# Kernel optimization log

Measured on AMD Instinct MI355X. Metric: run time of the kernel, lower is better.

Reference implementation:

```python
import jax, jax.numpy as jnp
import numpy as np

T, B, V, E, H = 512, 64, 50000, 256, 256  # seq, batch, vocab, embed, lstm_hidden
D2 = 2 * H
NC = 5


def setup_inputs() -> dict:
    key = jax.random.key(0)
    ks = jax.random.split(key, 16)
    u = lambda k, shape, s=0.1: jax.random.uniform(k, shape, jnp.float32, -s, s)
    return {
        "embed": jax.random.randint(ks[0], (T, B), 0, V),
        "h0": jnp.zeros((2, B, H), jnp.float32),
        "c0": jnp.zeros((2, B, H), jnp.float32),
        "emb_table": jax.random.normal(ks[1], (V, E), jnp.float32),
        "Wih_f": u(ks[2], (4 * H, E)),
        "Whh_f": u(ks[3], (4 * H, H)),
        "bih_f": u(ks[4], (4 * H,)),
        "bhh_f": u(ks[5], (4 * H,)),
        "Wih_b": u(ks[6], (4 * H, E)),
        "Whh_b": u(ks[7], (4 * H, H)),
        "bih_b": u(ks[8], (4 * H,)),
        "bhh_b": u(ks[9], (4 * H,)),
        "W_word": u(ks[10], (D2, D2)),
        "b_word": u(ks[11], (D2,)),
        "proj_word": u(ks[12], (D2,)),
        "lin_W": u(ks[13], (NC, D2)),
        "lin_b": u(ks[14], (NC,)),
    }


def _lstm_dir(x, h0, c0, Wih, Whh, bih, bhh):
    # x: (T,B,E). PyTorch LSTM gate order: i, f, g, o.
    xg = jnp.einsum('tbe,ge->tbg', x, Wih) + bih + bhh  # (T,B,4H)

    def step(carry, xt):
        h, c = carry
        g = xt + h @ Whh.T
        i, f, gg, o = jnp.split(g, 4, axis=-1)
        c = jax.nn.sigmoid(f) * c + jax.nn.sigmoid(i) * jnp.tanh(gg)
        h = jax.nn.sigmoid(o) * jnp.tanh(c)
        return (h, c), h

    _, hs = jax.lax.scan(step, (h0, c0), xg)
    return hs  # (T,B,H)


def reference(embed, h0, c0, emb_table,
              Wih_f, Whh_f, bih_f, bhh_f,
              Wih_b, Whh_b, bih_b, bhh_b,
              W_word, b_word, proj_word, lin_W, lin_b):
    x = emb_table[embed]  # (T,B,E)
    out_f = _lstm_dir(x, h0[0], c0[0], Wih_f, Whh_f, bih_f, bhh_f)
    out_b = _lstm_dir(x[::-1], h0[1], c0[1], Wih_b, Whh_b, bih_b, bhh_b)[::-1]
    out = jnp.concatenate([out_f, out_b], axis=-1)  # (T,B,2H)
    # additive attention: tanh(out @ W + b) @ proj, softmax over T
    squish = jnp.tanh(jnp.einsum('tbd,de->tbe', out, W_word) + b_word)
    attn = jax.nn.softmax(jnp.einsum('tbd,d->tb', squish, proj_word), axis=0)
    vec = jnp.einsum('tb,tbd->bd', attn, out)  # (B,2H)
    return vec @ lin_W.T + lin_b  # (B, n_classes)
```

## Files before the change

kernel.cpp:

```cpp
#include <hip/hip_runtime.h>
#include <hip/hip_fp16.h>
#include <cstdint>
#include <cstddef>

#define TT 512
#define BB 64
#define EE 256
#define HH 256
#define G4 1024
#define DD 512
#define NCLS 5
#define CH 64
#define NCH (TT / CH)

typedef _Float16 half8 __attribute__((ext_vector_type(8)));
typedef float f32x4 __attribute__((ext_vector_type(4)));

#define OFF_XGF   0ull
#define OFF_XGB   8388608ull
#define OFF_OUTB  16777216ull
#define OFF_WHHF  50331648ull
#define OFF_WIHF  51380224ull
#define OFF_BIAS  52428800ull
#define OFF_HST   52436992ull
#define OFF_CST   52568064ull
#define OFF_LOG   52699136ull
#define OFF_ATT   52830208ull
#define OFF_HEX   52961280ull
#define OFF_FLG   53092352ull

__device__ __forceinline__ f32x4 mfma16(half8 a, half8 b, f32x4 c) {
  return __builtin_amdgcn_mfma_f32_16x16x32_f16(a, b, c, 0, 0, 0);
}
__device__ __forceinline__ float sigm(float x) {
  return __fdividef(1.f, 1.f + __expf(-x));
}
__device__ __forceinline__ float tanh_(float x) {
  float e = __expf(2.f * x);
  return 1.f - __fdividef(2.f, e + 1.f);
}
__device__ __forceinline__ f32x4 shflx4(f32x4 v, int mask) {
  f32x4 r;
  r[0] = __shfl_xor(v[0], mask, 64);
  r[1] = __shfl_xor(v[1], mask, 64);
  r[2] = __shfl_xor(v[2], mask, 64);
  r[3] = __shfl_xor(v[3], mask, 64);
  return r;
}

#define HSWZ(br, u) ((((br) * 256) + (u)) ^ (((br) & 7) << 3))

__global__ __launch_bounds__(256) void make_frags(
    const float* __restrict__ WhhF, const float* __restrict__ WhhB,
    const float* __restrict__ WihF, const float* __restrict__ WihB,
    __half* __restrict__ whhfrag, __half* __restrict__ wihfrag)
{
  int idx = blockIdx.x * 256 + threadIdx.x;
  int r = idx & 7, lane = (idx >> 3) & 63, ks = (idx >> 9) & 7;
  int mm = lane & 15;
  int k = ks * 32 + (lane >> 4) * 8 + r;
  if (idx < (1 << 19)) {
    int pf = (idx >> 12) & 63, d = (idx >> 18) & 1;
    const float* W = d ? WhhB : WhhF;
    int g = (mm & 3) * 256 + pf * 4 + (mm >> 2);
    whhfrag[idx] = __float2half(W[(size_t)g * HH + k]);
  } else {
    int e = idx - (1 << 19);
    int pf = (e >> 12) & 63, d = (e >> 18) & 1;
    const float* W = d ? WihB : WihF;
    int g = (mm & 3) * 256 + pf * 4 + (mm >> 2);
    wihfrag[e] = __float2half(W[(size_t)g * EE + k]);
  }
}

__global__ __launch_bounds__(256) void bias_prep(
    const float* __restrict__ bihF, const float* __restrict__ bhhF,
    const float* __restrict__ bihB, const float* __restrict__ bhhB,
    float* __restrict__ bias)
{
  int i = blockIdx.x * 256 + threadIdx.x;
  int d = i >> 10, pcol = i & 1023;
  int g = (pcol & 3) * 256 + (pcol >> 2);
  bias[i] = (d ? bihB : bihF)[g] + (d ? bhhB : bhhF)[g];
}

__global__ __launch_bounds__(256) void xg_mfma(
    int c, const int* __restrict__ embed, const float* __restrict__ emb,
    const __half* __restrict__ wihfrag, const float* __restrict__ biassum,
    __half* __restrict__ xgF, __half* __restrict__ xgB)
{
  const int d = blockIdx.z, ls = blockIdx.x, gblk = blockIdx.y;
  int t = c * CH + ls;
  if (d) t = TT - 1 - t;
  __half* xg = d ? xgB : xgF;
  const int tid = threadIdx.x, w = tid >> 6, l = tid & 63;

  __shared__ int idx[64];
  __shared__ unsigned short xs[64 * 256];

  if (tid < 64) idx[tid] = embed[t * BB + tid];
  __syncthreads();

  {
    const int rr = tid >> 2, cq = (tid & 3) * 64;
    const float* src = emb + (size_t)idx[rr] * EE + cq;
#pragma unroll
    for (int j = 0; j < 8; ++j) {
      float4 a = *(const float4*)(src + j * 8);
      float4 b = *(const float4*)(src + j * 8 + 4);
      half8 hv;
      hv[0] = (_Float16)a.x; hv[1] = (_Float16)a.y; hv[2] = (_Float16)a.z; hv[3] = (_Float16)a.w;
      hv[4] = (_Float16)b.x; hv[5] = (_Float16)b.y; hv[6] = (_Float16)b.z; hv[7] = (_Float16)b.w;
      int hidx = (rr * 256 + cq + j * 8) ^ ((rr & 7) << 3);
      *(half8*)&xs[hidx] = hv;
    }
  }
  __syncthreads();

  const __half* bfb = wihfrag + (size_t)((d * 64 + gblk * 4) * 8) * 512 + l * 8;
  half8 Bf[4][8];
#pragma unroll
  for (int ct = 0; ct < 4; ++ct)
#pragma unroll
    for (int ks = 0; ks < 8; ++ks)
      Bf[ct][ks] = *(const half8*)(bfb + (ct * 8 + ks) * 512);

  f32x4 acc[4];
#pragma unroll
  for (int ct = 0; ct < 4; ++ct) {
    float bv = biassum[d * 1024 + gblk * 64 + ct * 16 + (l & 15)];
    acc[ct][0] = bv; acc[ct][1] = bv; acc[ct][2] = bv; acc[ct][3] = bv;
  }

  const int arow = w * 16 + (l & 15);
#pragma unroll
  for (int ks = 0; ks < 8; ++ks) {
    int hidx = (arow * 256 + ks * 32 + (l >> 4) * 8) ^ ((arow & 7) << 3);
    half8 af = *(const half8*)&xs[hidx];
#pragma unroll
    for (int ct = 0; ct < 4; ++ct)
      acc[ct] = mfma16(af, Bf[ct][ks], acc[ct]);
  }

#pragma unroll
  for (int ct = 0; ct < 4; ++ct) {
    ushort4 sv;
    sv.x = __half_as_ushort(__float2half(acc[ct][0]));
    sv.y = __half_as_ushort(__float2half(acc[ct][1]));
    sv.z = __half_as_ushort(__float2half(acc[ct][2]));
    sv.w = __half_as_ushort(__float2half(acc[ct][3]));
    size_t base = ((size_t)(ls * 4 + w) * 64 + (gblk * 4 + ct)) * 256 + l * 4;
    *(ushort4*)((unsigned short*)xg + base) = sv;
  }
}

__global__ __launch_bounds__(512, 2) void scan_dist(
    int c, const __half* __restrict__ xgF, const __half* __restrict__ xgB,
    const __half* __restrict__ whhfrag,
    const float* __restrict__ hin, const float* __restrict__ cin,
    float* __restrict__ hstate, float* __restrict__ cstate,
    __half* __restrict__ outb, __half* __restrict__ hex, int* __restrict__ flags)
{
  const int d = blockIdx.y;
  const int bg = blockIdx.x >> 2, ug = blockIdx.x & 3;
  const int tid = threadIdx.x, w = tid >> 6, l = tid & 63;
  const int m = l & 15, qr = l >> 4, q = m & 3, ul = m >> 2;
  const unsigned short* xg = (const unsigned short*)(d ? xgB : xgF);

  __shared__ unsigned short hb[16 * 256];

  const int pf0 = ug * 16 + w * 2;

  half8 Wf[2][8];
#pragma unroll
  for (int cf = 0; cf < 2; ++cf)
#pragma unroll
    for (int ks = 0; ks < 8; ++ks)
      Wf[cf][ks] = *(const half8*)(whhfrag +
          ((size_t)(d * 64 + pf0 + cf) * 8 + ks) * 512 + l * 8);

#pragma unroll
  for (int i = 0; i < 8; ++i) {
    int idx = i * 512 + tid;
    int r = idx >> 8, u = idx & 255;
    hb[HSWZ(r, u)] = __half_as_ushort(
        __float2half(hin[(size_t)(d * BB + bg * 16 + r) * HH + u]));
  }
  float cst[2][4];
#pragma unroll
  for (int cf = 0; cf < 2; ++cf) {
    int U = (pf0 + cf) * 4 + ul;
#pragma unroll
    for (int j = 0; j < 4; ++j)
      cst[cf][j] = cin[(size_t)(d * BB + bg * 16 + qr * 4 + j) * HH + U];
  }
  __syncthreads();

  const int pr = tid >> 5;
  const int uL = (tid & 31) * 2;

  for (int ls = 0; ls < CH; ++ls) {
    int t = c * CH + ls;
    if (d) t = TT - 1 - t;

    ushort4 xv[2];
#pragma unroll
    for (int cf = 0; cf < 2; ++cf) {
      size_t base = ((size_t)(ls * 4 + bg) * 64 + (pf0 + cf)) * 256 + l * 4;
      xv[cf] = *(const ushort4*)(xg + base);
    }
    half8 af[8];
#pragma unroll
    for (int ks = 0; ks < 8; ++ks)
      af[ks] = *(const half8*)&hb[HSWZ(m, ks * 32 + qr * 8)];
    __syncthreads();

    f32x4 acc[2];
#pragma unroll
    for (int cf = 0; cf < 2; ++cf) {
      acc[cf][0] = __half2float(__ushort_as_half(xv[cf].x));
      acc[cf][1] = __half2float(__ushort_as_half(xv[cf].y));
      acc[cf][2] = __half2float(__ushort_as_half(xv[cf].z));
      acc[cf][3] = __half2float(__ushort_as_half(xv[cf].w));
    }
#pragma unroll
    for (int ks = 0; ks < 8; ++ks)
#pragma unroll
      for (int cf = 0; cf < 2; ++cf)
        acc[cf] = mfma16(af[ks], Wf[cf][ks], acc[cf]);

#pragma unroll
    for (int cf = 0; cf < 2; ++cf) {
      f32x4 e = acc[cf];
      f32x4 o1 = shflx4(e, 1);
      f32x4 gev = (q & 1) ? o1 : e;
      f32x4 gov = (q & 1) ? e : o1;
      f32x4 ge2 = shflx4(gev, 2);
      f32x4 go2 = shflx4(gov, 2);
      f32x4 gi = (q & 2) ? ge2 : gev;
      f32x4 gg = (q & 2) ? gev : ge2;
      f32x4 gf = (q & 2) ? go2 : gov;
      f32x4 go = (q & 2) ? gov : go2;
      int U = (pf0 + cf) * 4 + ul;
#pragma unroll
      for (int j = 0; j < 4; ++j) {
        float ig = sigm(gi[j]), fg = sigm(gf[j]);
        float gz = tanh_(gg[j]), og = sigm(go[j]);
        cst[cf][j] = fg * cst[cf][j] + ig * gz;
        float hv = og * tanh_(cst[cf][j]);
        if (q == 0) {
          int r = qr * 4 + j;
          hb[HSWZ(r, U)] = __half_as_ushort(__float2half(hv));
        }
      }
    }
    __syncthreads();

    unsigned int* hexu =
        (unsigned int*)hex + (size_t)(d * 2 + (ls & 1)) * (64 * 256 / 2);
    {
      int u = ug * 64 + uL;
      unsigned int v = *(const unsigned int*)&hb[HSWZ(pr, u)];
      __hip_atomic_store(&hexu[((bg * 16 + pr) * 256 + u) >> 1], v,
                         __ATOMIC_RELAXED, __HIP_MEMORY_SCOPE_AGENT);
      *(unsigned int*)&outb[((size_t)t * BB + bg * 16 + pr) * DD + d * HH + u] =
          v;
    }
    asm volatile("s_waitcnt vmcnt(0)" ::: "memory");
    __syncthreads();
    const int fbase = (((d * NCH + c) * CH + ls) * 4 + bg) * 4;
    if (tid == 0)
      __hip_atomic_store(&flags[fbase + ug], 1, __ATOMIC_RELAXED,
                         __HIP_MEMORY_SCOPE_AGENT);
    if (tid < 4 && tid != ug) {
      while (__hip_atomic_load(&flags[fbase + tid], __ATOMIC_RELAXED,
                               __HIP_MEMORY_SCOPE_AGENT) == 0)
        __builtin_amdgcn_s_sleep(1);
    }
    asm volatile("" ::: "memory");
    __syncthreads();

#pragma unroll
    for (int p = 0; p < 3; ++p) {
      int peer = p + (p >= ug ? 1 : 0);
      int u = peer * 64 + uL;
      unsigned int pv =
          __hip_atomic_load(&hexu[((bg * 16 + pr) * 256 + u) >> 1],
                            __ATOMIC_RELAXED, __HIP_MEMORY_SCOPE_AGENT);
      *(unsigned int*)&hb[HSWZ(pr, u)] = pv;
    }
    __syncthreads();
  }

#pragma unroll
  for (int i = 0; i < 8; ++i) {
    int idx = i * 512 + tid;
    int r = idx >> 8, u = idx & 255;
    hstate[(size_t)(d * BB + bg * 16 + r) * HH + u] =
        __half2float(__ushort_as_half(hb[HSWZ(r, u)]));
  }
  if (q == 0) {
#pragma unroll
    for (int cf = 0; cf < 2; ++cf) {
      int U = (pf0 + cf) * 4 + ul;
#pragma unroll
      for (int j = 0; j < 4; ++j)
        cstate[(size_t)(d * BB + bg * 16 + qr * 4 + j) * HH + U] = cst[cf][j];
    }
  }
}

__global__ __launch_bounds__(1024, 1) void squish_logits(
    const __half* __restrict__ outb, const float* __restrict__ Ww,
    const float* __restrict__ bw, const float* __restrict__ proj,
    float* __restrict__ logits)
{
  const int r0 = blockIdx.x * 64;
  const int tid = threadIdx.x;
  const int tm = tid >> 6;
  const int tn = tid & 63;
  __shared__ float As[16][68];
  __shared__ float Bs[16][516];
  __shared__ float red[64][65];

  float acc[4][8] = {};
  const int am = tid >> 4, ak = tid & 15;
  const int bk = tid >> 7, bn = (tid & 127) * 4;

  for (int k0 = 0; k0 < DD; k0 += 16) {
    float a0 = __half2float(outb[(size_t)(r0 + am) * DD + k0 + ak]);
    float4 b0 = *(const float4*)&Ww[(size_t)(k0 + bk) * DD + bn];
    float4 b1 = *(const float4*)&Ww[(size_t)(k0 + bk + 8) * DD + bn];
    __syncthreads();
    As[ak][am] = a0;
    *(float4*)&Bs[bk][bn] = b0;
    *(float4*)&Bs[bk + 8][bn] = b1;
    __syncthreads();
#pragma unroll
    for (int k = 0; k < 16; ++k) {
      float4 a = *(const float4*)&As[k][tm * 4];
      float4 p0 = *(const float4*)&Bs[k][tn * 8];
      float4 p1 = *(const float4*)&Bs[k][tn * 8 + 4];
      float av[4] = {a.x, a.y, a.z, a.w};
#pragma unroll
      for (int i = 0; i < 4; ++i) {
        acc[i][0] += av[i] * p0.x; acc[i][1] += av[i] * p0.y;
        acc[i][2] += av[i] * p0.z; acc[i][3] += av[i] * p0.w;
        acc[i][4] += av[i] * p1.x; acc[i][5] += av[i] * p1.y;
        acc[i][6] += av[i] * p1.z; acc[i][7] += av[i] * p1.w;
      }
    }
  }
  float partial[4] = {0.f, 0.f, 0.f, 0.f};
#pragma unroll
  for (int jj = 0; jj < 8; ++jj) {
    int col = tn * 8 + jj;
    float bwv = bw[col], pv = proj[col];
#pragma unroll
    for (int i = 0; i < 4; ++i)
      partial[i] += tanhf(acc[i][jj] + bwv) * pv;
  }
#pragma unroll
  for (int i = 0; i < 4; ++i) red[tm * 4 + i][tn] = partial[i];
  __syncthreads();
  if (tid < 64) {
    float s = 0.f;
    for (int x = 0; x < 64; ++x) s += red[tid][x];
    logits[r0 + tid] = s;
  }
}

__global__ __launch_bounds__(256) void softmax_t(const float* __restrict__ logits,
                                                 float* __restrict__ attn)
{
  const int b = blockIdx.x;
  const int tid = threadIdx.x;
  __shared__ float sm[256];
  float v0 = logits[tid * BB + b];
  float v1 = logits[(tid + 256) * BB + b];
  sm[tid] = fmaxf(v0, v1);
  __syncthreads();
  for (int s = 128; s > 0; s >>= 1) {
    if (tid < s) sm[tid] = fmaxf(sm[tid], sm[tid + s]);
    __syncthreads();
  }
  float M = sm[0];
  __syncthreads();
  float e0 = expf(v0 - M), e1 = expf(v1 - M);
  sm[tid] = e0 + e1;
  __syncthreads();
  for (int s = 128; s > 0; s >>= 1) {
    if (tid < s) sm[tid] += sm[tid + s];
    __syncthreads();
  }
  float inv = 1.f / sm[0];
  attn[tid * BB + b] = e0 * inv;
  attn[(tid + 256) * BB + b] = e1 * inv;
}

__global__ __launch_bounds__(512) void vec_final(
    const __half* __restrict__ outb, const float* __restrict__ attn,
    const float* __restrict__ linW, const float* __restrict__ linb,
    float* __restrict__ y)
{
  const int b = blockIdx.x;
  const int d = threadIdx.x;
  float acc = 0.f;
  for (int t = 0; t < TT; ++t)
    acc += attn[t * BB + b] * __half2float(outb[((size_t)t * BB + b) * DD + d]);
  __shared__ float red[512];
  for (int cls = 0; cls < NCLS; ++cls) {
    red[d] = acc * linW[cls * DD + d];
    __syncthreads();
    for (int s = 256; s > 0; s >>= 1) {
      if (d < s) red[d] += red[d + s];
      __syncthreads();
    }
    if (d == 0) y[b * NCLS + cls] = red[0] + linb[cls];
    __syncthreads();
  }
}

extern "C" void kernel_launch(void* const* d_in, const int* in_sizes, int n_in,
                              void* d_out, int out_size, void* d_ws, size_t ws_size,
                              hipStream_t stream) {
  const int*   embed     = (const int*)d_in[0];
  const float* h0        = (const float*)d_in[1];
  const float* c0        = (const float*)d_in[2];
  const float* emb_table = (const float*)d_in[3];
  const float* Wih_f     = (const float*)d_in[4];
  const float* Whh_f     = (const float*)d_in[5];
  const float* bih_f     = (const float*)d_in[6];
  const float* bhh_f     = (const float*)d_in[7];
  const float* Wih_b     = (const float*)d_in[8];
  const float* Whh_b     = (const float*)d_in[9];
  const float* bih_b     = (const float*)d_in[10];
  const float* bhh_b     = (const float*)d_in[11];
  const float* W_word    = (const float*)d_in[12];
  const float* b_word    = (const float*)d_in[13];
  const float* proj_word = (const float*)d_in[14];
  const float* lin_W     = (const float*)d_in[15];
  const float* lin_b     = (const float*)d_in[16];

  char* ws = (char*)d_ws;
  __half* xgF     = (__half*)(ws + OFF_XGF);
  __half* xgB     = (__half*)(ws + OFF_XGB);
  __half* outb    = (__half*)(ws + OFF_OUTB);
  __half* whhfrag = (__half*)(ws + OFF_WHHF);
  __half* wihfrag = (__half*)(ws + OFF_WIHF);
  float*  biassum = (float*)(ws + OFF_BIAS);
  float*  hstate  = (float*)(ws + OFF_HST);
  float*  cstate  = (float*)(ws + OFF_CST);
  float*  logits  = (float*)(ws + OFF_LOG);
  float*  attn    = (float*)(ws + OFF_ATT);
  __half* hex     = (__half*)(ws + OFF_HEX);
  int*    flags   = (int*)(ws + OFF_FLG);

  hipMemsetAsync(flags, 0, 65536, stream);

  make_frags<<<4096, 256, 0, stream>>>(Whh_f, Whh_b, Wih_f, Wih_b, whhfrag, wihfrag);
  bias_prep<<<8, 256, 0, stream>>>(bih_f, bhh_f, bih_b, bhh_b, biassum);

  for (int c = 0; c < NCH; ++c) {
    xg_mfma<<<dim3(CH, 16, 2), 256, 0, stream>>>(c, embed, emb_table,
        wihfrag, biassum, xgF, xgB);
    const float* hin = (c == 0) ? h0 : hstate;
    const float* cin = (c == 0) ? c0 : cstate;
    scan_dist<<<dim3(16, 2), 512, 0, stream>>>(c, xgF, xgB, whhfrag,
        hin, cin, hstate, cstate, outb, hex, flags);
  }

  squish_logits<<<512, 1024, 0, stream>>>(outb, W_word, b_word, proj_word, logits);
  softmax_t<<<64, 256, 0, stream>>>(logits, attn);
  vec_final<<<64, 512, 0, stream>>>(outb, attn, lin_W, lin_b, (float*)d_out);
}
```

Before: 3.375 ms.

## Interleave two batch groups per scan block and fuse gate activations

The recurrent LSTM scan kernel now gives each block two batch groups, so two independent recurrences interleave their MFMA and activation latency, and the grid shrinks from 32 to 16 blocks. Each lane now computes its own gate activation with one exp-based formula before the shuffles, and the hidden-exchange buffer is relaid out so results are published right after compute. The kernel also prefetches the next step's input gates and moves the output write after the exchange. In exchange, each step does twice the work per block on half as many CUs, with more registers and shared memory per block.

```diff
diff --git a/kernel.cpp b/kernel.cpp
--- a/kernel.cpp
+++ b/kernel.cpp
@@ -154,7 +154,7 @@
   }
 }
 
-__global__ __launch_bounds__(512, 2) void scan_dist(
+__global__ __launch_bounds__(512, 2) void scan_dist2(
     int c, const __half* __restrict__ xgF, const __half* __restrict__ xgB,
     const __half* __restrict__ whhfrag,
     const float* __restrict__ hin, const float* __restrict__ cin,
@@ -162,12 +162,14 @@
     __half* __restrict__ outb, __half* __restrict__ hex, int* __restrict__ flags)
 {
   const int d = blockIdx.y;
-  const int bg = blockIdx.x >> 2, ug = blockIdx.x & 3;
+  const int bp = blockIdx.x >> 2, ug = blockIdx.x & 3;
   const int tid = threadIdx.x, w = tid >> 6, l = tid & 63;
   const int m = l & 15, qr = l >> 4, q = m & 3, ul = m >> 2;
+  const int bgA = bp * 2, bgB = bp * 2 + 1;
   const unsigned short* xg = (const unsigned short*)(d ? xgB : xgF);
 
-  __shared__ unsigned short hb[16 * 256];
+  __shared__ unsigned short hbA[16 * 256];
+  __shared__ unsigned short hbB[16 * 256];
 
   const int pf0 = ug * 16 + w * 2;
 
@@ -183,129 +185,186 @@
   for (int i = 0; i < 8; ++i) {
     int idx = i * 512 + tid;
     int r = idx >> 8, u = idx & 255;
-    hb[HSWZ(r, u)] = __half_as_ushort(
-        __float2half(hin[(size_t)(d * BB + bg * 16 + r) * HH + u]));
-  }
-  float cst[2][4];
+    hbA[HSWZ(r, u)] = __half_as_ushort(
+        __float2half(hin[(size_t)(d * BB + bgA * 16 + r) * HH + u]));
+    hbB[HSWZ(r, u)] = __half_as_ushort(
+        __float2half(hin[(size_t)(d * BB + bgB * 16 + r) * HH + u]));
+  }
+  float cstA[2][4], cstB[2][4];
 #pragma unroll
   for (int cf = 0; cf < 2; ++cf) {
     int U = (pf0 + cf) * 4 + ul;
 #pragma unroll
-    for (int j = 0; j < 4; ++j)
-      cst[cf][j] = cin[(size_t)(d * BB + bg * 16 + qr * 4 + j) * HH + U];
-  }
-  __syncthreads();
-
-  const int pr = tid >> 5;
-  const int uL = (tid & 31) * 2;
+    for (int j = 0; j < 4; ++j) {
+      cstA[cf][j] = cin[(size_t)(d * BB + bgA * 16 + qr * 4 + j) * HH + U];
+      cstB[cf][j] = cin[(size_t)(d * BB + bgB * 16 + qr * 4 + j) * HH + U];
+    }
+  }
+  __syncthreads();
+
+  int afo[8];
+#pragma unroll
+  for (int ks = 0; ks < 8; ++ks) afo[ks] = HSWZ(m, ks * 32 + qr * 8);
+
+  const unsigned short* xpA = xg + ((size_t)bgA * 64 + pf0) * 256 + l * 4;
+  const unsigned short* xpB = xpA + 16384;
+  ushort4 xvA[2], xvB[2];
+#pragma unroll
+  for (int cf = 0; cf < 2; ++cf) {
+    xvA[cf] = *(const ushort4*)(xpA + cf * 256);
+    xvB[cf] = *(const ushort4*)(xpB + cf * 256);
+  }
+
+  const float actB = (q == 2) ? 2.f : 1.f;
+  unsigned int* hexu = (unsigned int*)hex;
 
   for (int ls = 0; ls < CH; ++ls) {
-    int t = c * CH + ls;
-    if (d) t = TT - 1 - t;
-
-    ushort4 xv[2];
-#pragma unroll
-    for (int cf = 0; cf < 2; ++cf) {
-      size_t base = ((size_t)(ls * 4 + bg) * 64 + (pf0 + cf)) * 256 + l * 4;
-      xv[cf] = *(const ushort4*)(xg + base);
-    }
-    half8 af[8];
-#pragma unroll
-    for (int ks = 0; ks < 8; ++ks)
-      af[ks] = *(const half8*)&hb[HSWZ(m, ks * 32 + qr * 8)];
-    __syncthreads();
-
-    f32x4 acc[2];
-#pragma unroll
-    for (int cf = 0; cf < 2; ++cf) {
-      acc[cf][0] = __half2float(__ushort_as_half(xv[cf].x));
-      acc[cf][1] = __half2float(__ushort_as_half(xv[cf].y));
-      acc[cf][2] = __half2float(__ushort_as_half(xv[cf].z));
-      acc[cf][3] = __half2float(__ushort_as_half(xv[cf].w));
-    }
-#pragma unroll
-    for (int ks = 0; ks < 8; ++ks)
-#pragma unroll
-      for (int cf = 0; cf < 2; ++cf)
-        acc[cf] = mfma16(af[ks], Wf[cf][ks], acc[cf]);
-
-#pragma unroll
-    for (int cf = 0; cf < 2; ++cf) {
-      f32x4 e = acc[cf];
-      f32x4 o1 = shflx4(e, 1);
-      f32x4 gev = (q & 1) ? o1 : e;
-      f32x4 gov = (q & 1) ? e : o1;
-      f32x4 ge2 = shflx4(gev, 2);
-      f32x4 go2 = shflx4(gov, 2);
-      f32x4 gi = (q & 2) ? ge2 : gev;
-      f32x4 gg = (q & 2) ? gev : ge2;
-      f32x4 gf = (q & 2) ? go2 : gov;
-      f32x4 go = (q & 2) ? gov : go2;
-      int U = (pf0 + cf) * 4 + ul;
-#pragma unroll
-      for (int j = 0; j < 4; ++j) {
-        float ig = sigm(gi[j]), fg = sigm(gf[j]);
-        float gz = tanh_(gg[j]), og = sigm(go[j]);
-        cst[cf][j] = fg * cst[cf][j] + ig * gz;
-        float hv = og * tanh_(cst[cf][j]);
-        if (q == 0) {
-          int r = qr * 4 + j;
-          hb[HSWZ(r, U)] = __half_as_ushort(__float2half(hv));
-        }
+    int tA = c * CH + ls;
+    if (d) tA = TT - 1 - tA;
+    unsigned int* hx = hexu + (size_t)(d * 2 + (ls & 1)) * (256 * 32);
+
+    half8 afA[8], afB[8];
+#pragma unroll
+    for (int ks = 0; ks < 8; ++ks) {
+      afA[ks] = *(const half8*)&hbA[afo[ks]];
+      afB[ks] = *(const half8*)&hbB[afo[ks]];
+    }
+    __syncthreads();
+
+#define RING_COMPUTE(xv, af, cst, hbX, bgX)                                  \
+    {                                                                        \
+      f32x4 acc[2];                                                          \
+      _Pragma("unroll") for (int cf = 0; cf < 2; ++cf) {                     \
+        acc[cf][0] = __half2float(__ushort_as_half(xv[cf].x));               \
+        acc[cf][1] = __half2float(__ushort_as_half(xv[cf].y));               \
+        acc[cf][2] = __half2float(__ushort_as_half(xv[cf].z));               \
+        acc[cf][3] = __half2float(__ushort_as_half(xv[cf].w));               \
+      }                                                                      \
+      _Pragma("unroll") for (int ks = 0; ks < 8; ++ks)                       \
+        _Pragma("unroll") for (int cf = 0; cf < 2; ++cf)                     \
+          acc[cf] = mfma16(af[ks], Wf[cf][ks], acc[cf]);                     \
+      _Pragma("unroll") for (int cf = 0; cf < 2; ++cf) {                     \
+        f32x4 a0;                                                            \
+        _Pragma("unroll") for (int jj = 0; jj < 4; ++jj) {                   \
+          float e = __expf(actB * acc[cf][jj]);                              \
+          a0[jj] = 1.f - __fdividef(actB, e + 1.f);                          \
+        }                                                                    \
+        f32x4 a1 = shflx4(a0, 1);                                            \
+        f32x4 a2 = shflx4(a0, 2);                                            \
+        f32x4 a3 = shflx4(a0, 3);                                            \
+        const int U = (pf0 + cf) * 4 + ul;                                   \
+        float hv[4];                                                         \
+        _Pragma("unroll") for (int jj = 0; jj < 4; ++jj) {                   \
+          float cn = a1[jj] * cst[cf][jj] + a0[jj] * a2[jj];                 \
+          cst[cf][jj] = cn;                                                  \
+          float e2 = __expf(2.f * cn);                                       \
+          hv[jj] = a3[jj] * (1.f - __fdividef(2.f, e2 + 1.f));               \
+        }                                                                    \
+        if (q == 0) {                                                        \
+          unsigned int p0 = (unsigned int)__half_as_ushort(__float2half(hv[0])) |  \
+              ((unsigned int)__half_as_ushort(__float2half(hv[1])) << 16);   \
+          unsigned int p1 = (unsigned int)__half_as_ushort(__float2half(hv[2])) |  \
+              ((unsigned int)__half_as_ushort(__float2half(hv[3])) << 16);   \
+          hbX[HSWZ(qr * 4 + 0, U)] = (unsigned short)(p0 & 0xffff);          \
+          hbX[HSWZ(qr * 4 + 1, U)] = (unsigned short)(p0 >> 16);             \
+          hbX[HSWZ(qr * 4 + 2, U)] = (unsigned short)(p1 & 0xffff);          \
+          hbX[HSWZ(qr * 4 + 3, U)] = (unsigned short)(p1 >> 16);             \
+          int rpb = U * 32 + bgX * 8 + qr * 2;                               \
+          __hip_atomic_store(&hx[rpb], p0, __ATOMIC_RELAXED,                 \
+                             __HIP_MEMORY_SCOPE_AGENT);                      \
+          __hip_atomic_store(&hx[rpb + 1], p1, __ATOMIC_RELAXED,             \
+                             __HIP_MEMORY_SCOPE_AGENT);                      \
+        }                                                                    \
+      }                                                                      \
+    }
+
+    RING_COMPUTE(xvA, afA, cstA, hbA, bgA)
+    RING_COMPUTE(xvB, afB, cstB, hbB, bgB)
+
+    asm volatile("s_waitcnt vmcnt(0)" ::: "memory");
+    __syncthreads();
+    const int fb = (((d * NCH + c) * CH + ls) * 4) * 4;
+    if (tid == 0) {
+      __hip_atomic_store(&flags[fb + bgA * 4 + ug], 1, __ATOMIC_RELAXED,
+                         __HIP_MEMORY_SCOPE_AGENT);
+      __hip_atomic_store(&flags[fb + bgB * 4 + ug], 1, __ATOMIC_RELAXED,
+                         __HIP_MEMORY_SCOPE_AGENT);
+    }
+    if (tid < 4) {
+      if (tid != ug) {
+        while (__hip_atomic_load(&flags[fb + bgA * 4 + tid], __ATOMIC_RELAXED,
+                                 __HIP_MEMORY_SCOPE_AGENT) == 0)
+          __builtin_amdgcn_s_sleep(1);
       }
-    }
-    __syncthreads();
-
-    unsigned int* hexu =
-        (unsigned int*)hex + (size_t)(d * 2 + (ls & 1)) * (64 * 256 / 2);
+    } else if (tid < 8) {
+      int pg = tid - 4;
+      if (pg != ug) {
+        while (__hip_atomic_load(&flags[fb + bgB * 4 + pg], __ATOMIC_RELAXED,
+                                 __HIP_MEMORY_SCOPE_AGENT) == 0)
+          __builtin_amdgcn_s_sleep(1);
+      }
+    }
+    asm volatile("" ::: "memory");
+    __syncthreads();
+
     {
-      int u = ug * 64 + uL;
-      unsigned int v = *(const unsigned int*)&hb[HSWZ(pr, u)];
-      __hip_atomic_store(&hexu[((bg * 16 + pr) * 256 + u) >> 1], v,
-                         __ATOMIC_RELAXED, __HIP_MEMORY_SCOPE_AGENT);
-      *(unsigned int*)&outb[((size_t)t * BB + bg * 16 + pr) * DD + d * HH + u] =
-          v;
-    }
-    asm volatile("s_waitcnt vmcnt(0)" ::: "memory");
-    __syncthreads();
-    const int fbase = (((d * NCH + c) * CH + ls) * 4 + bg) * 4;
-    if (tid == 0)
-      __hip_atomic_store(&flags[fbase + ug], 1, __ATOMIC_RELAXED,
-                         __HIP_MEMORY_SCOPE_AGENT);
-    if (tid < 4 && tid != ug) {
-      while (__hip_atomic_load(&flags[fbase + tid], __ATOMIC_RELAXED,
-                               __HIP_MEMORY_SCOPE_AGENT) == 0)
-        __builtin_amdgcn_s_sleep(1);
-    }
-    asm volatile("" ::: "memory");
-    __syncthreads();
-
-#pragma unroll
-    for (int p = 0; p < 3; ++p) {
-      int peer = p + (p >= ug ? 1 : 0);
-      int u = peer * 64 + uL;
-      unsigned int pv =
-          __hip_atomic_load(&hexu[((bg * 16 + pr) * 256 + u) >> 1],
-                            __ATOMIC_RELAXED, __HIP_MEMORY_SCOPE_AGENT);
-      *(unsigned int*)&hb[HSWZ(pr, u)] = pv;
-    }
-    __syncthreads();
+      const int uu = tid >> 3, rl2 = tid & 7;
+#pragma unroll
+      for (int p = 0; p < 3; ++p) {
+        int peer = p + (p >= ug ? 1 : 0);
+        int U = peer * 64 + uu;
+        unsigned int vA = __hip_atomic_load(&hx[U * 32 + bgA * 8 + rl2],
+                                            __ATOMIC_RELAXED,
+                                            __HIP_MEMORY_SCOPE_AGENT);
+        hbA[HSWZ(rl2 * 2 + 0, U)] = (unsigned short)(vA & 0xffff);
+        hbA[HSWZ(rl2 * 2 + 1, U)] = (unsigned short)(vA >> 16);
+        unsigned int vB = __hip_atomic_load(&hx[U * 32 + bgB * 8 + rl2],
+                                            __ATOMIC_RELAXED,
+                                            __HIP_MEMORY_SCOPE_AGENT);
+        hbB[HSWZ(rl2 * 2 + 0, U)] = (unsigned short)(vB & 0xffff);
+        hbB[HSWZ(rl2 * 2 + 1, U)] = (unsigned short)(vB >> 16);
+      }
+    }
+    {
+      const int pr = tid >> 5, uL = (tid & 31) * 2;
+      const int u = ug * 64 + uL;
+      *(unsigned int*)&outb[((size_t)tA * BB + bgA * 16 + pr) * DD + d * HH + u] =
+          *(const unsigned int*)&hbA[HSWZ(pr, u)];
+      *(unsigned int*)&outb[((size_t)tA * BB + bgB * 16 + pr) * DD + d * HH + u] =
+          *(const unsigned int*)&hbB[HSWZ(pr, u)];
+    }
+    {
+      int lsn = (ls + 1 < CH) ? ls + 1 : ls;
+      const unsigned short* xA = xpA + (size_t)lsn * 65536;
+      const unsigned short* xB = xpB + (size_t)lsn * 65536;
+#pragma unroll
+      for (int cf = 0; cf < 2; ++cf) {
+        xvA[cf] = *(const ushort4*)(xA + cf * 256);
+        xvB[cf] = *(const ushort4*)(xB + cf * 256);
+      }
+    }
+    __syncthreads();
+#undef RING_COMPUTE
   }
 
 #pragma unroll
   for (int i = 0; i < 8; ++i) {
     int idx = i * 512 + tid;
     int r = idx >> 8, u = idx & 255;
-    hstate[(size_t)(d * BB + bg * 16 + r) * HH + u] =
-        __half2float(__ushort_as_half(hb[HSWZ(r, u)]));
+    hstate[(size_t)(d * BB + bgA * 16 + r) * HH + u] =
+        __half2float(__ushort_as_half(hbA[HSWZ(r, u)]));
+    hstate[(size_t)(d * BB + bgB * 16 + r) * HH + u] =
+        __half2float(__ushort_as_half(hbB[HSWZ(r, u)]));
   }
   if (q == 0) {
 #pragma unroll
     for (int cf = 0; cf < 2; ++cf) {
       int U = (pf0 + cf) * 4 + ul;
 #pragma unroll
-      for (int j = 0; j < 4; ++j)
-        cstate[(size_t)(d * BB + bg * 16 + qr * 4 + j) * HH + U] = cst[cf][j];
+      for (int j = 0; j < 4; ++j) {
+        cstate[(size_t)(d * BB + bgA * 16 + qr * 4 + j) * HH + U] = cstA[cf][j];
+        cstate[(size_t)(d * BB + bgB * 16 + qr * 4 + j) * HH + U] = cstB[cf][j];
+      }
     }
   }
 }
@@ -466,7 +525,7 @@
         wihfrag, biassum, xgF, xgB);
     const float* hin = (c == 0) ? h0 : hstate;
     const float* cin = (c == 0) ? c0 : cstate;
-    scan_dist<<<dim3(16, 2), 512, 0, stream>>>(c, xgF, xgB, whhfrag,
+    scan_dist2<<<dim3(8, 2), 512, 0, stream>>>(c, xgF, xgB, whhfrag,
         hin, cin, hstate, cstate, outb, hex, flags);
   }
 
```

Result: slower. 3.617 ms (+7.2%).

## Overlap own-slice MFMA with peer exchange and streamline LSTM gate activations

Applied to the files above, without the earlier changes.

The scan kernel now computes the matmul contribution of its own h slice for the next step before waiting on peer flags, and prefetches xg two steps ahead. This takes part of the MFMA work and the global load latency off the cross-block synchronization critical path. Gate activations use a single unified exp/divide form, where the sigmoid is written via a scaled tanh expression, followed by three shuffles instead of the select-heavy shuffle tree. The h exchange writes go straight from registers, dropping one barrier. Block-to-index mapping, exchange layout and flag sizing change as well, which enlarges the flag memset.

```diff
diff --git a/kernel.cpp b/kernel.cpp
--- a/kernel.cpp
+++ b/kernel.cpp
@@ -31,13 +31,6 @@
 
 __device__ __forceinline__ f32x4 mfma16(half8 a, half8 b, f32x4 c) {
   return __builtin_amdgcn_mfma_f32_16x16x32_f16(a, b, c, 0, 0, 0);
-}
-__device__ __forceinline__ float sigm(float x) {
-  return __fdividef(1.f, 1.f + __expf(-x));
-}
-__device__ __forceinline__ float tanh_(float x) {
-  float e = __expf(2.f * x);
-  return 1.f - __fdividef(2.f, e + 1.f);
 }
 __device__ __forceinline__ f32x4 shflx4(f32x4 v, int mask) {
   f32x4 r;
@@ -154,15 +147,16 @@
   }
 }
 
-__global__ __launch_bounds__(512, 2) void scan_dist(
+__global__ __launch_bounds__(512, 2) void scan_dist3(
     int c, const __half* __restrict__ xgF, const __half* __restrict__ xgB,
     const __half* __restrict__ whhfrag,
     const float* __restrict__ hin, const float* __restrict__ cin,
     float* __restrict__ hstate, float* __restrict__ cstate,
     __half* __restrict__ outb, __half* __restrict__ hex, int* __restrict__ flags)
 {
-  const int d = blockIdx.y;
-  const int bg = blockIdx.x >> 2, ug = blockIdx.x & 3;
+  const int id = blockIdx.x;
+  const int ug = id >> 3, grp = id & 7;
+  const int d = grp >> 2, bg = grp & 3;
   const int tid = threadIdx.x, w = tid >> 6, l = tid & 63;
   const int m = l & 15, qr = l >> 4, q = m & 3, ul = m >> 2;
   const unsigned short* xg = (const unsigned short*)(d ? xgB : xgF);
@@ -196,26 +190,112 @@
   }
   __syncthreads();
 
-  const int pr = tid >> 5;
-  const int uL = (tid & 31) * 2;
+  int afo[8];
+#pragma unroll
+  for (int ks = 0; ks < 8; ++ks) afo[ks] = HSWZ(m, ks * 32 + qr * 8);
+  const int kso0 = ug * 2, kso1 = ug * 2 + 1;
+
+  const unsigned short* xp = xg + ((size_t)bg * 64 + pf0) * 256 + l * 4;
+
+  unsigned int* hexu = (unsigned int*)hex;
+  const float actB = (q == 2) ? 2.f : 1.f;
+
+  f32x4 acc[2];
+  {
+    ushort4 xv0[2];
+#pragma unroll
+    for (int cf = 0; cf < 2; ++cf) xv0[cf] = *(const ushort4*)(xp + cf * 256);
+#pragma unroll
+    for (int cf = 0; cf < 2; ++cf) {
+      acc[cf][0] = __half2float(__ushort_as_half(xv0[cf].x));
+      acc[cf][1] = __half2float(__ushort_as_half(xv0[cf].y));
+      acc[cf][2] = __half2float(__ushort_as_half(xv0[cf].z));
+      acc[cf][3] = __half2float(__ushort_as_half(xv0[cf].w));
+    }
+    half8 ao0 = *(const half8*)&hb[afo[kso0]];
+    half8 ao1 = *(const half8*)&hb[afo[kso1]];
+#pragma unroll
+    for (int cf = 0; cf < 2; ++cf) {
+      acc[cf] = mfma16(ao0, Wf[cf][kso0], acc[cf]);
+      acc[cf] = mfma16(ao1, Wf[cf][kso1], acc[cf]);
+    }
+  }
+  ushort4 xv[2];
+#pragma unroll
+  for (int cf = 0; cf < 2; ++cf)
+    xv[cf] = *(const ushort4*)(xp + (size_t)65536 + cf * 256);
 
   for (int ls = 0; ls < CH; ++ls) {
-    int t = c * CH + ls;
-    if (d) t = TT - 1 - t;
-
-    ushort4 xv[2];
+    int tA = c * CH + ls;
+    if (d) tA = TT - 1 - tA;
+    unsigned int* hx = hexu + (size_t)(grp * 2 + (ls & 1)) * 2048;
+
+    half8 afp[6];
+#pragma unroll
+    for (int i = 0; i < 6; ++i) {
+      int ks = i + (i >= kso0 ? 2 : 0);
+      afp[i] = *(const half8*)&hb[afo[ks]];
+    }
+    __syncthreads();
+
+#pragma unroll
+    for (int i = 0; i < 6; ++i) {
+      int ks = i + (i >= kso0 ? 2 : 0);
+#pragma unroll
+      for (int cf = 0; cf < 2; ++cf)
+        acc[cf] = mfma16(afp[i], Wf[cf][ks], acc[cf]);
+    }
+
 #pragma unroll
     for (int cf = 0; cf < 2; ++cf) {
-      size_t base = ((size_t)(ls * 4 + bg) * 64 + (pf0 + cf)) * 256 + l * 4;
-      xv[cf] = *(const ushort4*)(xg + base);
-    }
-    half8 af[8];
-#pragma unroll
-    for (int ks = 0; ks < 8; ++ks)
-      af[ks] = *(const half8*)&hb[HSWZ(m, ks * 32 + qr * 8)];
-    __syncthreads();
-
-    f32x4 acc[2];
+      f32x4 a0;
+#pragma unroll
+      for (int jj = 0; jj < 4; ++jj) {
+        float e = __expf(actB * acc[cf][jj]);
+        a0[jj] = 1.f - __fdividef(actB, e + 1.f);
+      }
+      f32x4 a1 = shflx4(a0, 1);
+      f32x4 a2 = shflx4(a0, 2);
+      f32x4 a3 = shflx4(a0, 3);
+      const int U = (pf0 + cf) * 4 + ul;
+      float hv[4];
+#pragma unroll
+      for (int jj = 0; jj < 4; ++jj) {
+        float cn = a1[jj] * cst[cf][jj] + a0[jj] * a2[jj];
+        cst[cf][jj] = cn;
+        float e2 = __expf(2.f * cn);
+        hv[jj] = a3[jj] * (1.f - __fdividef(2.f, e2 + 1.f));
+      }
+      if (q == 0) {
+        unsigned int p0 = (unsigned int)__half_as_ushort(__float2half(hv[0])) |
+            ((unsigned int)__half_as_ushort(__float2half(hv[1])) << 16);
+        unsigned int p1 = (unsigned int)__half_as_ushort(__float2half(hv[2])) |
+            ((unsigned int)__half_as_ushort(__float2half(hv[3])) << 16);
+        hb[HSWZ(qr * 4 + 0, U)] = (unsigned short)(p0 & 0xffff);
+        hb[HSWZ(qr * 4 + 1, U)] = (unsigned short)(p0 >> 16);
+        hb[HSWZ(qr * 4 + 2, U)] = (unsigned short)(p1 & 0xffff);
+        hb[HSWZ(qr * 4 + 3, U)] = (unsigned short)(p1 >> 16);
+        int rpb = U * 8 + qr * 2;
+        __hip_atomic_store(&hx[rpb], p0, __ATOMIC_RELAXED,
+                           __HIP_MEMORY_SCOPE_AGENT);
+        __hip_atomic_store(&hx[rpb + 1], p1, __ATOMIC_RELAXED,
+                           __HIP_MEMORY_SCOPE_AGENT);
+      }
+    }
+    asm volatile("s_waitcnt vmcnt(0)" ::: "memory");
+    __syncthreads();
+
+    const int fbase = (((grp * NCH + c) * CH + ls)) * 32;
+    if (tid == 0)
+      __hip_atomic_store(&flags[fbase + ug], 1, __ATOMIC_RELAXED,
+                         __HIP_MEMORY_SCOPE_AGENT);
+
+    {
+      const int pr = tid >> 5, uL = (tid & 31) * 2;
+      const int u = ug * 64 + uL;
+      *(unsigned int*)&outb[((size_t)tA * BB + bg * 16 + pr) * DD + d * HH + u] =
+          *(const unsigned int*)&hb[HSWZ(pr, u)];
+    }
 #pragma unroll
     for (int cf = 0; cf < 2; ++cf) {
       acc[cf][0] = __half2float(__ushort_as_half(xv[cf].x));
@@ -223,55 +303,22 @@
       acc[cf][2] = __half2float(__ushort_as_half(xv[cf].z));
       acc[cf][3] = __half2float(__ushort_as_half(xv[cf].w));
     }
-#pragma unroll
-    for (int ks = 0; ks < 8; ++ks)
+    {
+      half8 ao0 = *(const half8*)&hb[afo[kso0]];
+      half8 ao1 = *(const half8*)&hb[afo[kso1]];
+#pragma unroll
+      for (int cf = 0; cf < 2; ++cf) {
+        acc[cf] = mfma16(ao0, Wf[cf][kso0], acc[cf]);
+        acc[cf] = mfma16(ao1, Wf[cf][kso1], acc[cf]);
+      }
+    }
+    {
+      int lsn = (ls + 2 < CH) ? ls + 2 : CH - 1;
+      const unsigned short* xn = xp + (size_t)lsn * 65536;
 #pragma unroll
       for (int cf = 0; cf < 2; ++cf)
-        acc[cf] = mfma16(af[ks], Wf[cf][ks], acc[cf]);
-
-#pragma unroll
-    for (int cf = 0; cf < 2; ++cf) {
-      f32x4 e = acc[cf];
-      f32x4 o1 = shflx4(e, 1);
-      f32x4 gev = (q & 1) ? o1 : e;
-      f32x4 gov = (q & 1) ? e : o1;
-      f32x4 ge2 = shflx4(gev, 2);
-      f32x4 go2 = shflx4(gov, 2);
-      f32x4 gi = (q & 2) ? ge2 : gev;
-      f32x4 gg = (q & 2) ? gev : ge2;
-      f32x4 gf = (q & 2) ? go2 : gov;
-      f32x4 go = (q & 2) ? gov : go2;
-      int U = (pf0 + cf) * 4 + ul;
-#pragma unroll
-      for (int j = 0; j < 4; ++j) {
-        float ig = sigm(gi[j]), fg = sigm(gf[j]);
-        float gz = tanh_(gg[j]), og = sigm(go[j]);
-        cst[cf][j] = fg * cst[cf][j] + ig * gz;
-        float hv = og * tanh_(cst[cf][j]);
-        if (q == 0) {
-          int r = qr * 4 + j;
-          hb[HSWZ(r, U)] = __half_as_ushort(__float2half(hv));
-        }
-      }
-    }
-    __syncthreads();
-
-    unsigned int* hexu =
-        (unsigned int*)hex + (size_t)(d * 2 + (ls & 1)) * (64 * 256 / 2);
-    {
-      int u = ug * 64 + uL;
-      unsigned int v = *(const unsigned int*)&hb[HSWZ(pr, u)];
-      __hip_atomic_store(&hexu[((bg * 16 + pr) * 256 + u) >> 1], v,
-                         __ATOMIC_RELAXED, __HIP_MEMORY_SCOPE_AGENT);
-      *(unsigned int*)&outb[((size_t)t * BB + bg * 16 + pr) * DD + d * HH + u] =
-          v;
-    }
-    asm volatile("s_waitcnt vmcnt(0)" ::: "memory");
-    __syncthreads();
-    const int fbase = (((d * NCH + c) * CH + ls) * 4 + bg) * 4;
-    if (tid == 0)
-      __hip_atomic_store(&flags[fbase + ug], 1, __ATOMIC_RELAXED,
-                         __HIP_MEMORY_SCOPE_AGENT);
+        xv[cf] = *(const ushort4*)(xn + cf * 256);
+    }
     if (tid < 4 && tid != ug) {
       while (__hip_atomic_load(&flags[fbase + tid], __ATOMIC_RELAXED,
                                __HIP_MEMORY_SCOPE_AGENT) == 0)
@@ -280,14 +327,17 @@
     asm volatile("" ::: "memory");
     __syncthreads();
 
-#pragma unroll
-    for (int p = 0; p < 3; ++p) {
-      int peer = p + (p >= ug ? 1 : 0);
-      int u = peer * 64 + uL;
-      unsigned int pv =
-          __hip_atomic_load(&hexu[((bg * 16 + pr) * 256 + u) >> 1],
-                            __ATOMIC_RELAXED, __HIP_MEMORY_SCOPE_AGENT);
-      *(unsigned int*)&hb[HSWZ(pr, u)] = pv;
+    {
+      const int uu = tid >> 3, rl2 = tid & 7;
+#pragma unroll
+      for (int p = 0; p < 3; ++p) {
+        int peer = p + (p >= ug ? 1 : 0);
+        int U = peer * 64 + uu;
+        unsigned int v = __hip_atomic_load(&hx[U * 8 + rl2], __ATOMIC_RELAXED,
+                                           __HIP_MEMORY_SCOPE_AGENT);
+        hb[HSWZ(rl2 * 2 + 0, U)] = (unsigned short)(v & 0xffff);
+        hb[HSWZ(rl2 * 2 + 1, U)] = (unsigned short)(v >> 16);
+      }
     }
     __syncthreads();
   }
@@ -456,7 +506,7 @@
   __half* hex     = (__half*)(ws + OFF_HEX);
   int*    flags   = (int*)(ws + OFF_FLG);
 
-  hipMemsetAsync(flags, 0, 65536, stream);
+  hipMemsetAsync(flags, 0, 524288, stream);
 
   make_frags<<<4096, 256, 0, stream>>>(Whh_f, Whh_b, Wih_f, Wih_b, whhfrag, wihfrag);
   bias_prep<<<8, 256, 0, stream>>>(bih_f, bhh_f, bih_b, bhh_b, biassum);
@@ -466,7 +516,7 @@
         wihfrag, biassum, xgF, xgB);
     const float* hin = (c == 0) ? h0 : hstate;
     const float* cin = (c == 0) ? c0 : cstate;
-    scan_dist<<<dim3(16, 2), 512, 0, stream>>>(c, xgF, xgB, whhfrag,
+    scan_dist3<<<dim3(32), 512, 0, stream>>>(c, xgF, xgB, whhfrag,
         hin, cin, hstate, cstate, outb, hex, flags);
   }
 
```

Result: faster. 2.972 ms (-11.9%).
